# Kernel optimization log

Measured on AMD Instinct MI355X. Metric: run time of the kernel, lower is better.

The kernel has to match this reference:

```python
import jax, jax.numpy as jnp
import numpy as np

TAU = 0.5
THRESHOLD = 1.0
V_RESET = 0.0


def setup_inputs() -> dict:
    key = jax.random.key(0)
    T, B, D = 512, 64, 1024
    x = jax.random.normal(key, (T, B, D), dtype=jnp.float32)
    v0 = jnp.zeros((D,), dtype=jnp.float32)  # initial membrane potential, broadcasts over batch
    return {"x": x, "v0": v0}


def reference(x, v0):
    # x: [T, B, D] input current per timestep; v0: [D] initial potential.
    # Faithful LIF update per timestep: v = tau*v + x; spike = (v >= thr);
    # v = v*(1-spike) + v_reset*spike.  Sequential state carried by lax.scan.
    B, D = x.shape[1], x.shape[2]
    v_init = jnp.broadcast_to(v0, (B, D))

    def step(v, xt):
        v = TAU * v + xt
        spike = (v >= THRESHOLD).astype(xt.dtype)
        v = v * (1.0 - spike) + V_RESET * spike
        return v, spike

    _, spikes = jax.lax.scan(step, v_init, x)
    return spikes  # [T, B, D]
```

## Files before the change

### kernel.cpp

```cpp
#include <hip/hip_runtime.h>


constexpr int T_STEPS  = 512;
constexpr int B_DIM    = 64;
constexpr int D_DIM    = 1024;
constexpr int N_CHAIN  = B_DIM * D_DIM;
constexpr int VEC      = 4;
constexpr int NT_VEC   = N_CHAIN / VEC;
constexpr int C_CHUNKS = 4;
constexpr int T_CHUNK  = T_STEPS / C_CHUNKS;
constexpr int K_WARM   = 64;

typedef float v4f __attribute__((ext_vector_type(4)));

__global__ __launch_bounds__(256)
void lif_scan_kernel(const float* __restrict__ x,
                     const float* __restrict__ v0,
                     float* __restrict__ out) {
    const int col   = ((blockIdx.x & 63) << 8) + threadIdx.x;
    const int chunk = blockIdx.x >> 6;

    const v4f* xp = (const v4f*)x   + col;
    v4f*       op = (v4f*)      out + col;

    const int d0 = (col * VEC) & (D_DIM - 1);

    float v[VEC];
    const int tstart = chunk * T_CHUNK;

    if (chunk == 0) {
        const v4f vi = *(const v4f*)(v0 + d0);
        v[0] = vi.x; v[1] = vi.y; v[2] = vi.z; v[3] = vi.w;
    } else {
#pragma unroll
        for (int i = 0; i < VEC; ++i) v[i] = 0.0f;
#pragma unroll 16
        for (int t = tstart - K_WARM; t < tstart; ++t) {
            const v4f xv = xp[(size_t)t * NT_VEC];
            const float xs[VEC] = {xv.x, xv.y, xv.z, xv.w};
#pragma unroll
            for (int i = 0; i < VEC; ++i) {
                float vi = v[i] * 0.5f + xs[i];
                v[i] = (vi >= 1.0f) ? 0.0f : vi;
            }
        }
    }

#pragma unroll 16
    for (int t = tstart; t < tstart + T_CHUNK; ++t) {
        const v4f xv = xp[(size_t)t * NT_VEC];
        const float xs[VEC] = {xv.x, xv.y, xv.z, xv.w};
        float ss[VEC];
#pragma unroll
        for (int i = 0; i < VEC; ++i) {
            float vi = v[i] * 0.5f + xs[i];
            const bool sp = (vi >= 1.0f);
            ss[i] = sp ? 1.0f : 0.0f;
            v[i]  = sp ? 0.0f : vi;
        }
        v4f s;
        s.x = ss[0]; s.y = ss[1]; s.z = ss[2]; s.w = ss[3];
        __builtin_nontemporal_store(s, op + (size_t)t * NT_VEC);
    }
}

extern "C" void kernel_launch(void* const* d_in, const int* in_sizes, int n_in,
                              void* d_out, int out_size, void* d_ws, size_t ws_size,
                              hipStream_t stream) {
    const float* x   = (const float*)d_in[0];
    const float* v0  = (const float*)d_in[1];
    float*       out = (float*)d_out;

    dim3 block(256);
    dim3 grid(C_CHUNKS * (NT_VEC / 256));
    hipLaunchKernelGGL(lif_scan_kernel, grid, block, 0, stream, x, v0, out);
}
```

Before: 238.5 us.

## Double-buffer global loads with inline asm and manual vmcnt waits

Replaces the simple per-timestep load/compute loops with a software pipeline. Eight timesteps of input are loaded into one register buffer while the other buffer is consumed. Inline-asm global loads and explicit s_waitcnt vmcnt barriers keep many loads in flight per thread. This targets the latency-bound behaviour of the low-occupancy grid. It raises register use and relies on hand-counted vmcnt values that must account for outstanding stores.

```diff
diff --git a/kernel.cpp b/kernel.cpp
--- a/kernel.cpp
+++ b/kernel.cpp
@@ -10,10 +10,49 @@
 constexpr int C_CHUNKS = 4;
 constexpr int T_CHUNK  = T_STEPS / C_CHUNKS;
 constexpr int K_WARM   = 64;
+constexpr int U        = 8;
 
 typedef float v4f __attribute__((ext_vector_type(4)));
 
-__global__ __launch_bounds__(256)
+#define WAITV(N)                                                      \
+    do {                                                              \
+        asm volatile("s_waitcnt vmcnt(" #N ")" ::: "memory");         \
+        __builtin_amdgcn_sched_barrier(0);                            \
+    } while (0)
+
+__device__ __forceinline__ void load8(v4f (&buf)[U],
+                                      const v4f* __restrict__ xp, int tbase) {
+#pragma unroll
+    for (int k = 0; k < U; ++k)
+        asm volatile("global_load_dwordx4 %0, %1, off"
+                     : "=v"(buf[k])
+                     : "v"(xp + (size_t)(tbase + k) * NT_VEC)
+                     : "memory");
+}
+
+template<bool ST>
+__device__ __forceinline__ void cons8(const v4f (&buf)[U], float (&v)[VEC],
+                                      v4f* __restrict__ op, int tbase) {
+#pragma unroll
+    for (int k = 0; k < U; ++k) {
+        const float xs[VEC] = {buf[k].x, buf[k].y, buf[k].z, buf[k].w};
+        float ss[VEC];
+#pragma unroll
+        for (int i = 0; i < VEC; ++i) {
+            float vi = v[i] * 0.5f + xs[i];
+            const bool sp = (vi >= 1.0f);
+            ss[i] = sp ? 1.0f : 0.0f;
+            v[i]  = sp ? 0.0f : vi;
+        }
+        if (ST) {
+            v4f s;
+            s.x = ss[0]; s.y = ss[1]; s.z = ss[2]; s.w = ss[3];
+            __builtin_nontemporal_store(s, op + (size_t)(tbase + k) * NT_VEC);
+        }
+    }
+}
+
+__global__ __launch_bounds__(256, 1)
 void lif_scan_kernel(const float* __restrict__ x,
                      const float* __restrict__ v0,
                      float* __restrict__ out) {
@@ -22,46 +61,39 @@
 
     const v4f* xp = (const v4f*)x   + col;
     v4f*       op = (v4f*)      out + col;
-
-    const int d0 = (col * VEC) & (D_DIM - 1);
+    const int  d0 = (col * VEC) & (D_DIM - 1);
 
     float v[VEC];
+    v4f bA[U], bB[U];
     const int tstart = chunk * T_CHUNK;
 
     if (chunk == 0) {
         const v4f vi = *(const v4f*)(v0 + d0);
         v[0] = vi.x; v[1] = vi.y; v[2] = vi.z; v[3] = vi.w;
+        load8(bA, xp, tstart);
     } else {
 #pragma unroll
         for (int i = 0; i < VEC; ++i) v[i] = 0.0f;
-#pragma unroll 16
-        for (int t = tstart - K_WARM; t < tstart; ++t) {
-            const v4f xv = xp[(size_t)t * NT_VEC];
-            const float xs[VEC] = {xv.x, xv.y, xv.z, xv.w};
-#pragma unroll
-            for (int i = 0; i < VEC; ++i) {
-                float vi = v[i] * 0.5f + xs[i];
-                v[i] = (vi >= 1.0f) ? 0.0f : vi;
-            }
+        const int tw = tstart - K_WARM;
+        load8(bA, xp, tw);
+        for (int p = 0; p < 4; ++p) {
+            load8(bB, xp, tw + (2 * p + 1) * U); WAITV(8);
+            cons8<false>(bA, v, op, 0);
+            load8(bA, xp, tw + (2 * p + 2) * U); WAITV(8);
+            cons8<false>(bB, v, op, 0);
         }
     }
 
-#pragma unroll 16
-    for (int t = tstart; t < tstart + T_CHUNK; ++t) {
-        const v4f xv = xp[(size_t)t * NT_VEC];
-        const float xs[VEC] = {xv.x, xv.y, xv.z, xv.w};
-        float ss[VEC];
-#pragma unroll
-        for (int i = 0; i < VEC; ++i) {
-            float vi = v[i] * 0.5f + xs[i];
-            const bool sp = (vi >= 1.0f);
-            ss[i] = sp ? 1.0f : 0.0f;
-            v[i]  = sp ? 0.0f : vi;
-        }
-        v4f s;
-        s.x = ss[0]; s.y = ss[1]; s.z = ss[2]; s.w = ss[3];
-        __builtin_nontemporal_store(s, op + (size_t)t * NT_VEC);
+    load8(bB, xp, tstart + 1 * U);  WAITV(8);   cons8<true>(bA, v, op, tstart);
+    load8(bA, xp, tstart + 2 * U);  WAITV(16);  cons8<true>(bB, v, op, tstart + 1 * U);
+    for (int p = 1; p < 7; ++p) {
+        load8(bB, xp, tstart + (2 * p + 1) * U); WAITV(16);
+        cons8<true>(bA, v, op, tstart + (2 * p) * U);
+        load8(bA, xp, tstart + (2 * p + 2) * U); WAITV(16);
+        cons8<true>(bB, v, op, tstart + (2 * p + 1) * U);
     }
+    load8(bB, xp, tstart + 15 * U); WAITV(16);  cons8<true>(bA, v, op, tstart + 14 * U);
+    WAITV(8);                                   cons8<true>(bB, v, op, tstart + 15 * U);
 }
 
 extern "C" void kernel_launch(void* const* d_in, const int* in_sizes, int n_in,
```

After: 239.7 us. Within noise of the previous version (+0.5%).
